# Optimization experiments

Hardware: AMD Instinct MI355X
Metric: run time of the kernel (lower is better)

## Reference

```python
import jax, jax.numpy as jnp
import numpy as np


def setup_inputs() -> dict:
    key = jax.random.key(0)
    k1, k2, k3 = jax.random.split(key, 3)
    B, D, C = 512, 256, 1000
    embedding = jax.random.normal(k1, (B, D), dtype=jnp.float32)
    labels = jax.random.randint(k2, (B,), 0, C, dtype=jnp.int64)
    W = jax.random.normal(k3, (C, D), dtype=jnp.float32) * 0.02
    return {"embedding": embedding, "labels": labels, "W": W}


def reference(embedding, labels, W):
    # MRL-E loss: (1/D) * sum_{k=1..D} CE(z[:, :k] @ W[:, :k].T, y)
    # Computed incrementally: logits_k = logits_{k-1} + z[:, k] outer W[:, k],
    # which is mathematically identical to recomputing the prefix matmul.
    B, D = embedding.shape
    C = W.shape[0]
    rows = jnp.arange(B)
    labels = labels.astype(jnp.int32)

    def step(logits, cols):
        z_col, w_col = cols  # [B], [C]
        logits = logits + z_col[:, None] * w_col[None, :]  # rank-1 update, [B, C]
        # stable cross-entropy: mean(logsumexp(logits) - logits[i, y_i])
        lse = jax.nn.logsumexp(logits, axis=-1)  # [B]
        lab_logit = logits[rows, labels]  # [B]
        loss_k = jnp.mean(lse - lab_logit)
        return logits, loss_k

    init = jnp.zeros((B, C), dtype=embedding.dtype)
    _, losses = jax.lax.scan(step, init, (embedding.T, W.T))  # losses: [D]
    return jnp.sum(losses) / D
```

## Files before the change

kernel.cpp:

```cpp
#include <hip/hip_runtime.h>
#include <hip/hip_bf16.h>
#include <math.h>


#define MRLE_B 512
#define MRLE_D 256
#define MRLE_C 1000
#define MRLE_CP 1024
#define MRLE_KROWS 264
#define MRLE_NT 512
#define ROWD (MRLE_CP / 2)
#define LOG2E 1.4426950408889634f
#define LN2   0.6931471805599453f

#if __has_builtin(__builtin_amdgcn_exp2f)
#define EXP2(x) __builtin_amdgcn_exp2f(x)
#else
#define EXP2(x) __builtin_exp2f(x)
#endif

__global__ __launch_bounds__(256) void mrle_transpose(
    const float* __restrict__ W, unsigned short* __restrict__ Wtb)
{
    __shared__ float tile[64][65];
    const int c0 = blockIdx.x * 64;
    const int k0 = blockIdx.y * 64;
    const int t  = threadIdx.x;
    const int r  = t >> 2;
    const int q  = t & 3;

#pragma unroll
    for (int j = 0; j < 4; ++j) {
        const int c    = c0 + r;
        const int kcol = q * 4 + j * 16;
        float4 v = make_float4(0.f, 0.f, 0.f, 0.f);
        if (c < MRLE_C) v = *(const float4*)&W[(size_t)c * MRLE_D + k0 + kcol];
        tile[r][kcol + 0] = v.x;
        tile[r][kcol + 1] = v.y;
        tile[r][kcol + 2] = v.z;
        tile[r][kcol + 3] = v.w;
    }
    __syncthreads();

#pragma unroll
    for (int j = 0; j < 4; ++j) {
        const int cc = q * 4 + j * 16;
        unsigned short hh[4];
#pragma unroll
        for (int e = 0; e < 4; ++e) {
            const float f = tile[cc + e][r] * LOG2E;
            unsigned int u = __float_as_uint(f);
            u = (u + 0x7FFFu + ((u >> 16) & 1u)) >> 16;
            hh[e] = (unsigned short)u;
        }
        *(ushort4*)&Wtb[(size_t)(k0 + r) * MRLE_CP + c0 + cc] =
            make_ushort4(hh[0], hh[1], hh[2], hh[3]);
    }
}

__global__ __launch_bounds__(MRLE_NT) void mrle_main(
    const float* __restrict__ z,
    const int* __restrict__ labels,
    const float* __restrict__ W,
    const unsigned short* __restrict__ Wtb,
    float* __restrict__ out)
{
    __shared__ float zsh[MRLE_D];
    __shared__ float red[8 * 16 * 64];
    __shared__ float Sw[8 * MRLE_D];
    __shared__ float wred[8];

    const int i  = blockIdx.x;
    const int t  = threadIdx.x;
    const int wv = t >> 6;
    const int l  = t & 63;

    if (t < MRLE_D) zsh[t] = z[i * MRLE_D + t];
    __syncthreads();

    const int cbase = 2 * t;
    float l0 = (cbase     < MRLE_C) ? 0.f : -INFINITY;
    float l1 = (cbase + 1 < MRLE_C) ? 0.f : -INFINITY;

    const unsigned int* Wp = (const unsigned int*)Wtb + t;

    unsigned int wbuf[8];
#pragma unroll
    for (int q = 0; q < 8; ++q) wbuf[q] = Wp[(size_t)q * ROWD];

    float* redw = red + wv * (16 * 64);
    const int khat = l & 15;
    const int q16  = l & 48;

#pragma unroll 1
    for (int cb = 0; cb < 16; ++cb) {
        float zq[16];
        *(float4*)&zq[0]  = *(const float4*)&zsh[cb * 16 + 0];
        *(float4*)&zq[4]  = *(const float4*)&zsh[cb * 16 + 4];
        *(float4*)&zq[8]  = *(const float4*)&zsh[cb * 16 + 8];
        *(float4*)&zq[12] = *(const float4*)&zsh[cb * 16 + 12];

#pragma unroll
        for (int kk = 0; kk < 16; ++kk) {
            const int k = cb * 16 + kk;
            const unsigned int w = wbuf[kk & 7];
            const float w0 = __uint_as_float(w << 16);
            const float w1 = __uint_as_float(w & 0xFFFF0000u);
            l0 = fmaf(zq[kk], w0, l0);
            l1 = fmaf(zq[kk], w1, l1);
            redw[kk * 64 + ((l + kk) & 63)] = EXP2(l0) + EXP2(l1);
            wbuf[kk & 7] = Wp[(size_t)(k + 8) * ROWD];
        }

        float s = 0.f;
#pragma unroll
        for (int u = 0; u < 16; ++u)
            s += redw[khat * 64 + ((q16 + u + khat) & 63)];
        s += __shfl_xor(s, 16);
        s += __shfl_xor(s, 32);
        if (l < 16) Sw[wv * MRLE_D + cb * 16 + khat] = s;
    }

    __syncthreads();

    float v = 0.f;
    if (t < MRLE_D) {
        float S = 0.f;
#pragma unroll
        for (int wq = 0; wq < 8; ++wq) S += Sw[wq * MRLE_D + t];
        const float lse = LN2 * __log2f(S);

        const int y = labels[i];
        const float lab = zsh[t] * W[(size_t)y * MRLE_D + t] *
                          (float)(MRLE_D - t);
        v = lse - lab;
    }

#pragma unroll
    for (int d = 1; d < 64; d <<= 1) v += __shfl_xor(v, d);
    if (l == 0) wred[wv] = v;
    __syncthreads();
    if (t == 0) {
        float tot = 0.f;
#pragma unroll
        for (int wq = 0; wq < 8; ++wq) tot += wred[wq];
        atomicAdd(out, tot * (1.0f / ((float)MRLE_B * (float)MRLE_D)));
    }
}

extern "C" void kernel_launch(void* const* d_in, const int* in_sizes, int n_in,
                              void* d_out, int out_size, void* d_ws, size_t ws_size,
                              hipStream_t stream) {
    const float* z      = (const float*)d_in[0];
    const int*   labels = (const int*)d_in[1];
    const float* W      = (const float*)d_in[2];
    float*       out    = (float*)d_out;

    unsigned short* Wtb = (unsigned short*)d_ws;

    hipMemsetAsync(out, 0, sizeof(float), stream);
    mrle_transpose<<<dim3(16, 4), 256, 0, stream>>>(W, Wtb);
    mrle_main<<<MRLE_B, MRLE_NT, 0, stream>>>(z, labels, W, Wtb, out);
}
```

Before: 39.37 us.

## Compute prefix logits and exp-sums with fp16 MFMA instead of scalar FMAs

The per-step rank-1 logit updates become MFMA 16x16x32 fp16 matrix ops: masked triangular z operands produce all 32 prefix logits of a block at once, and a second MFMA against a ones vector does the exp-sum reduction instead of LDS shuffles. W is pre-permuted into fp16 in a simpler prep kernel that also zeroes the output, which drops the memset call. This removes scalar FMA and LDS reduction traffic. The cost is lower precision: fp16 for z, W, logits inputs and the exp values.

```diff
diff --git a/kernel.cpp b/kernel.cpp
--- a/kernel.cpp
+++ b/kernel.cpp
@@ -6,10 +6,6 @@
 #define MRLE_B 512
 #define MRLE_D 256
 #define MRLE_C 1000
-#define MRLE_CP 1024
-#define MRLE_KROWS 264
-#define MRLE_NT 512
-#define ROWD (MRLE_CP / 2)
 #define LOG2E 1.4426950408889634f
 #define LN2   0.6931471805599453f
 
@@ -19,54 +15,32 @@
 #define EXP2(x) __builtin_exp2f(x)
 #endif
 
-__global__ __launch_bounds__(256) void mrle_transpose(
-    const float* __restrict__ W, unsigned short* __restrict__ Wtb)
+typedef _Float16 half8 __attribute__((ext_vector_type(8)));
+typedef float    f32x4 __attribute__((ext_vector_type(4)));
+
+#define MFMA __builtin_amdgcn_mfma_f32_16x16x32_f16
+
+__global__ __launch_bounds__(256) void mrle_prep(
+    const float* __restrict__ W, _Float16* __restrict__ Wh,
+    float* __restrict__ out)
 {
-    __shared__ float tile[64][65];
-    const int c0 = blockIdx.x * 64;
-    const int k0 = blockIdx.y * 64;
-    const int t  = threadIdx.x;
-    const int r  = t >> 2;
-    const int q  = t & 3;
-
-#pragma unroll
-    for (int j = 0; j < 4; ++j) {
-        const int c    = c0 + r;
-        const int kcol = q * 4 + j * 16;
-        float4 v = make_float4(0.f, 0.f, 0.f, 0.f);
-        if (c < MRLE_C) v = *(const float4*)&W[(size_t)c * MRLE_D + k0 + kcol];
-        tile[r][kcol + 0] = v.x;
-        tile[r][kcol + 1] = v.y;
-        tile[r][kcol + 2] = v.z;
-        tile[r][kcol + 3] = v.w;
-    }
-    __syncthreads();
-
-#pragma unroll
-    for (int j = 0; j < 4; ++j) {
-        const int cc = q * 4 + j * 16;
-        unsigned short hh[4];
-#pragma unroll
-        for (int e = 0; e < 4; ++e) {
-            const float f = tile[cc + e][r] * LOG2E;
-            unsigned int u = __float_as_uint(f);
-            u = (u + 0x7FFFu + ((u >> 16) & 1u)) >> 16;
-            hh[e] = (unsigned short)u;
-        }
-        *(ushort4*)&Wtb[(size_t)(k0 + r) * MRLE_CP + c0 + cc] =
-            make_ushort4(hh[0], hh[1], hh[2], hh[3]);
-    }
+    const int c = blockIdx.x;
+    const int d = threadIdx.x;
+    if (c == 0 && d == 0) out[0] = 0.f;
+    const int kb = d >> 5, r5 = d & 31, g = r5 >> 3, e = r5 & 7;
+    const int k  = kb * 32 + g * 4 + (e & 3) + ((e >> 2) << 4);
+    float v = 0.f;
+    if (c < MRLE_C) v = W[c * MRLE_D + k] * LOG2E;
+    Wh[(size_t)c * MRLE_D + d] = (_Float16)v;
 }
 
-__global__ __launch_bounds__(MRLE_NT) void mrle_main(
+__global__ __launch_bounds__(512, 4) void mrle_main(
     const float* __restrict__ z,
     const int* __restrict__ labels,
     const float* __restrict__ W,
-    const unsigned short* __restrict__ Wtb,
+    const _Float16* __restrict__ Wh,
     float* __restrict__ out)
 {
-    __shared__ float zsh[MRLE_D];
-    __shared__ float red[8 * 16 * 64];
     __shared__ float Sw[8 * MRLE_D];
     __shared__ float wred[8];
 
@@ -74,51 +48,79 @@
     const int t  = threadIdx.x;
     const int wv = t >> 6;
     const int l  = t & 63;
+    const int lg = l >> 4;
+    const int ln = l & 15;
 
-    if (t < MRLE_D) zsh[t] = z[i * MRLE_D + t];
-    __syncthreads();
+    const float* zrow = z + (size_t)i * MRLE_D;
 
-    const int cbase = 2 * t;
-    float l0 = (cbase     < MRLE_C) ? 0.f : -INFINITY;
-    float l1 = (cbase + 1 < MRLE_C) ? 0.f : -INFINITY;
+    const _Float16* Abase = Wh + ((size_t)(wv * 128 + ln)) * MRLE_D + lg * 8;
 
-    const unsigned int* Wp = (const unsigned int*)Wtb + t;
+    f32x4 Lb[8];
+#pragma unroll
+    for (int c8 = 0; c8 < 8; ++c8) Lb[c8] = (f32x4){0.f, 0.f, 0.f, 0.f};
 
-    unsigned int wbuf[8];
+    const _Float16 H0 = (_Float16)0.f, H1 = (_Float16)1.f;
+    const half8 ONES = {H1, H1, H1, H1, H0, H0, H0, H0};
+
+    half8 abuf[4];
 #pragma unroll
-    for (int q = 0; q < 8; ++q) wbuf[q] = Wp[(size_t)q * ROWD];
-
-    float* redw = red + wv * (16 * 64);
-    const int khat = l & 15;
-    const int q16  = l & 48;
+    for (int p = 0; p < 4; ++p)
+        abuf[p] = *(const half8*)(Abase + (size_t)p * 4096);
 
 #pragma unroll 1
-    for (int cb = 0; cb < 16; ++cb) {
-        float zq[16];
-        *(float4*)&zq[0]  = *(const float4*)&zsh[cb * 16 + 0];
-        *(float4*)&zq[4]  = *(const float4*)&zsh[cb * 16 + 4];
-        *(float4*)&zq[8]  = *(const float4*)&zsh[cb * 16 + 8];
-        *(float4*)&zq[12] = *(const float4*)&zsh[cb * 16 + 12];
+    for (int kb = 0; kb < 8; ++kb) {
+        const float4 zlo = *(const float4*)&zrow[kb * 32 + lg * 4];
+        const float4 zhi = *(const float4*)&zrow[kb * 32 + 16 + lg * 4];
+        const _Float16 zl0 = (_Float16)zlo.x, zl1 = (_Float16)zlo.y,
+                       zl2 = (_Float16)zlo.z, zl3 = (_Float16)zlo.w;
+        const _Float16 zh0 = (_Float16)zhi.x, zh1 = (_Float16)zhi.y,
+                       zh2 = (_Float16)zhi.z, zh3 = (_Float16)zhi.w;
+        const bool m0 = (lg * 4 + 0) <= ln, m1 = (lg * 4 + 1) <= ln,
+                   m2 = (lg * 4 + 2) <= ln, m3 = (lg * 4 + 3) <= ln;
+        const half8 Ba = {m0 ? zl0 : H0, m1 ? zl1 : H0, m2 ? zl2 : H0,
+                          m3 ? zl3 : H0, H0, H0, H0, H0};
+        const half8 Bb = {zl0, zl1, zl2, zl3,
+                          m0 ? zh0 : H0, m1 ? zh1 : H0, m2 ? zh2 : H0,
+                          m3 ? zh3 : H0};
+        const half8 Bz = {zl0, zl1, zl2, zl3, zh0, zh1, zh2, zh3};
+
+        f32x4 D2a = (f32x4){0.f, 0.f, 0.f, 0.f};
+        f32x4 D2b = (f32x4){0.f, 0.f, 0.f, 0.f};
 
 #pragma unroll
-        for (int kk = 0; kk < 16; ++kk) {
-            const int k = cb * 16 + kk;
-            const unsigned int w = wbuf[kk & 7];
-            const float w0 = __uint_as_float(w << 16);
-            const float w1 = __uint_as_float(w & 0xFFFF0000u);
-            l0 = fmaf(zq[kk], w0, l0);
-            l1 = fmaf(zq[kk], w1, l1);
-            redw[kk * 64 + ((l + kk) & 63)] = EXP2(l0) + EXP2(l1);
-            wbuf[kk & 7] = Wp[(size_t)(k + 8) * ROWD];
+        for (int cti = 0; cti < 8; ++cti) {
+            const half8 A = abuf[cti & 3];
+            if (kb < 7 || cti < 4) {
+                const int itn = kb * 8 + cti + 4;
+                abuf[cti & 3] = *(const half8*)(Abase +
+                    (size_t)(itn & 7) * 4096 + (size_t)(itn >> 3) * 32);
+            }
+
+            const f32x4 d1a = MFMA(A, Ba, Lb[cti], 0, 0, 0);
+            const f32x4 d1b = MFMA(A, Bb, Lb[cti], 0, 0, 0);
+            Lb[cti] = MFMA(A, Bz, Lb[cti], 0, 0, 0);
+
+            float pa0 = EXP2(d1a[0]), pa1 = EXP2(d1a[1]),
+                  pa2 = EXP2(d1a[2]), pa3 = EXP2(d1a[3]);
+            float pb0 = EXP2(d1b[0]), pb1 = EXP2(d1b[1]),
+                  pb2 = EXP2(d1b[2]), pb3 = EXP2(d1b[3]);
+            if (wv == 7 && cti >= 6) {
+                const float m = (cti == 7 || lg >= 2) ? 0.f : 1.f;
+                pa0 *= m; pa1 *= m; pa2 *= m; pa3 *= m;
+                pb0 *= m; pb1 *= m; pb2 *= m; pb3 *= m;
+            }
+            const half8 Pa = {(_Float16)pa0, (_Float16)pa1, (_Float16)pa2,
+                              (_Float16)pa3, H0, H0, H0, H0};
+            const half8 Pb = {(_Float16)pb0, (_Float16)pb1, (_Float16)pb2,
+                              (_Float16)pb3, H0, H0, H0, H0};
+            D2a = MFMA(ONES, Pa, D2a, 0, 0, 0);
+            D2b = MFMA(ONES, Pb, D2b, 0, 0, 0);
         }
 
-        float s = 0.f;
-#pragma unroll
-        for (int u = 0; u < 16; ++u)
-            s += redw[khat * 64 + ((q16 + u + khat) & 63)];
-        s += __shfl_xor(s, 16);
-        s += __shfl_xor(s, 32);
-        if (l < 16) Sw[wv * MRLE_D + cb * 16 + khat] = s;
+        if (l < 16) {
+            Sw[wv * MRLE_D + kb * 32 + l]      = D2a[0];
+            Sw[wv * MRLE_D + kb * 32 + 16 + l] = D2b[0];
+        }
     }
 
     __syncthreads();
@@ -129,13 +131,11 @@
 #pragma unroll
         for (int wq = 0; wq < 8; ++wq) S += Sw[wq * MRLE_D + t];
         const float lse = LN2 * __log2f(S);
-
         const int y = labels[i];
-        const float lab = zsh[t] * W[(size_t)y * MRLE_D + t] *
+        const float lab = zrow[t] * W[(size_t)y * MRLE_D + t] *
                           (float)(MRLE_D - t);
         v = lse - lab;
     }
-
 #pragma unroll
     for (int d = 1; d < 64; d <<= 1) v += __shfl_xor(v, d);
     if (l == 0) wred[wv] = v;
@@ -156,9 +156,8 @@
     const float* W      = (const float*)d_in[2];
     float*       out    = (float*)d_out;
 
-    unsigned short* Wtb = (unsigned short*)d_ws;
+    _Float16* Wh = (_Float16*)d_ws;
 
-    hipMemsetAsync(out, 0, sizeof(float), stream);
-    mrle_transpose<<<dim3(16, 4), 256, 0, stream>>>(W, Wtb);
-    mrle_main<<<MRLE_B, MRLE_NT, 0, stream>>>(z, labels, W, Wtb, out);
+    mrle_prep<<<1024, 256, 0, stream>>>(W, Wh, out);
+    mrle_main<<<MRLE_B, 512, 0, stream>>>(z, labels, W, Wh, out);
 }
```

Measured after the change: 45.80 us. +16.3%, slower.
